# Kernel tuning notes

Measured on AMD Instinct MI355X. Metric: run time of the kernel, lower is better.

Reference implementation:

```python
import jax, jax.numpy as jnp
import numpy as np

N_NODES = 87381  # complete 4-ary tree of depth 9: (4**9 - 1) / 3
VOCAB = 32000
D_IN = 256
M_DIM = 256


def setup_inputs() -> dict:
    key = jax.random.key(0)
    ks = jax.random.split(key, 10)
    w = lambda k, s: jax.random.normal(k, s, dtype=jnp.float32) * 0.05
    return {
        "tokens": jax.random.randint(ks[0], (N_NODES,), 0, VOCAB),
        "branching": 4,
        "emb": w(ks[1], (VOCAB, D_IN)),
        "Wioux": w(ks[2], (D_IN, 3 * M_DIM)),
        "bioux": w(ks[3], (3 * M_DIM,)),
        "Wiouh": w(ks[4], (M_DIM, 3 * M_DIM)),
        "biouh": w(ks[5], (3 * M_DIM,)),
        "Wfx": w(ks[6], (D_IN, M_DIM)),
        "bfx": w(ks[7], (M_DIM,)),
        "Wfh": w(ks[8], (M_DIM, M_DIM)),
        "bfh": w(ks[9], (M_DIM,)),
    }


def _levels(n, b):
    # BFS level boundaries (start, size) for a complete b-ary tree with n nodes
    out, start, size = [], 0, 1
    while start < n:
        out.append((start, min(size, n - start)))
        start += size
        size *= b
    return out


def reference(tokens, branching, emb, Wioux, bioux, Wiouh, biouh, Wfx, bfx, Wfh, bfh):
    N = tokens.shape[0]
    b = int(branching)
    M = Wfh.shape[0]
    x = emb[tokens]                       # [N, D_IN] per-node inputs
    xiou = x @ Wioux + bioux              # [N, 3M] precomputed input gate terms
    xf = x @ Wfx + bfx                    # [N, M]
    h = jnp.zeros((N, M), x.dtype)
    c = jnp.zeros((N, M), x.dtype)
    for (s, sz) in reversed(_levels(N, b)):  # leaves -> root
        idx = jnp.arange(s, s + sz)
        child = idx[:, None] * b + 1 + jnp.arange(b)[None, :]   # [sz, b]
        valid = (child < N)[..., None].astype(x.dtype)          # [sz, b, 1]
        ci = jnp.where(child < N, child, 0)
        ch = h[ci] * valid                                      # [sz, b, M]
        cc = c[ci] * valid
        iou = xiou[idx] + ch.sum(axis=1) @ Wiouh + biouh        # [sz, 3M]
        i, o, u = jnp.split(iou, 3, axis=1)
        i, o, u = jax.nn.sigmoid(i), jax.nn.sigmoid(o), jnp.tanh(u)
        f = jax.nn.sigmoid(ch @ Wfh + bfh + xf[idx][:, None, :])  # [sz, b, M]
        c_new = i * u + jnp.sum(f * cc * valid, axis=1)
        h_new = o * jnp.tanh(c_new)
        c = c.at[idx].set(c_new)
        h = h.at[idx].set(h_new)
    return h  # hidden state of every node; root state is h[0]
```

## Files before the change

kernel.cpp:

```cpp
#include <hip/hip_runtime.h>
#include <cstdint>
#include <cstddef>

typedef _Float16 f16;
typedef __attribute__((ext_vector_type(8))) _Float16 half8;
typedef __attribute__((ext_vector_type(4))) _Float16 half4;
typedef __attribute__((ext_vector_type(8))) short short8;
typedef __attribute__((ext_vector_type(4))) float floatx4;
typedef __attribute__((ext_vector_type(8))) float floatx8;

__device__ __forceinline__ float rcp_(float x) { return __builtin_amdgcn_rcpf(x); }
__device__ __forceinline__ float sigm(float x) { return rcp_(1.f + __expf(-x)); }
__device__ __forceinline__ float tanh_(float x) { return 1.f - 2.f * rcp_(1.f + __expf(2.f * x)); }

__global__ __launch_bounds__(256) void gemm128d(
    const f16* __restrict__ A0, const f16* __restrict__ B0, f16* __restrict__ C0,
    int ldc0, int nt0, int tiles0,
    const f16* __restrict__ A1, const f16* __restrict__ B1, f16* __restrict__ C1,
    int ldc1, int nt1)
{
  const f16* A; const f16* BT; f16* C; int ldc_, mi, ni;
  int bid = blockIdx.x;
  if (bid < tiles0) { A = A0; BT = B0; C = C0; ldc_ = ldc0; mi = bid / nt0; ni = bid % nt0; }
  else { int r = bid - tiles0; A = A1; BT = B1; C = C1; ldc_ = ldc1; mi = r / nt1; ni = r % nt1; }
  const int m0 = mi * 128;
  const int n0 = ni * 128;

  __shared__ short lA[128 * 72];
  __shared__ short lB[128 * 72];
  const int t = threadIdx.x;
  const int wave = t >> 6;
  const int lane = t & 63;
  const int ln = lane & 15;
  const int quad = lane >> 4;
  const int wr = wave >> 1;
  const int wc = wave & 1;

  floatx4 acc[4][4];
#pragma unroll
  for (int i = 0; i < 4; ++i)
#pragma unroll
    for (int j = 0; j < 4; ++j) acc[i][j] = (floatx4){0.f, 0.f, 0.f, 0.f};

#pragma unroll
  for (int st = 0; st < 4; ++st) {
    const int k0 = st * 64;
#pragma unroll
    for (int i = 0; i < 4; ++i) {
      int chunk = t + 256 * i;
      int row = chunk >> 3;
      int cc = chunk & 7;
      *(short8*)&lA[row * 72 + cc * 8] =
          *(const short8*)(A + (size_t)(m0 + row) * 256 + k0 + cc * 8);
      *(short8*)&lB[row * 72 + cc * 8] =
          *(const short8*)(BT + (size_t)(n0 + row) * 256 + k0 + cc * 8);
    }
    __syncthreads();
#pragma unroll
    for (int ks = 0; ks < 2; ++ks) {
      const int kk = ks * 32 + quad * 8;
      half8 a[4], b[4];
#pragma unroll
      for (int rf = 0; rf < 4; ++rf)
        a[rf] = __builtin_bit_cast(half8,
            *(const short8*)&lA[(wr * 64 + rf * 16 + ln) * 72 + kk]);
#pragma unroll
      for (int cf = 0; cf < 4; ++cf)
        b[cf] = __builtin_bit_cast(half8,
            *(const short8*)&lB[(wc * 64 + cf * 16 + ln) * 72 + kk]);
#pragma unroll
      for (int rf = 0; rf < 4; ++rf)
#pragma unroll
        for (int cf = 0; cf < 4; ++cf)
          acc[rf][cf] = __builtin_amdgcn_mfma_f32_16x16x32_f16(
              a[rf], b[cf], acc[rf][cf], 0, 0, 0);
    }
    __syncthreads();
  }
#pragma unroll
  for (int rf = 0; rf < 4; ++rf)
#pragma unroll
    for (int cf = 0; cf < 4; ++cf)
#pragma unroll
      for (int r = 0; r < 4; ++r) {
        int row = m0 + wr * 64 + rf * 16 + quad * 4 + r;
        int col = n0 + wc * 64 + cf * 16 + ln;
        C[(size_t)row * ldc_ + col] = (f16)acc[rf][cf][r];
      }
}

__global__ __launch_bounds__(256) void prep(
    const float* __restrict__ emb, const float* __restrict__ Wioux,
    const float* __restrict__ Wfx, const float* __restrict__ Wiouh,
    const float* __restrict__ Wfh,
    f16* __restrict__ emb_h, f16* __restrict__ BTX,
    f16* __restrict__ WiouhT, f16* __restrict__ WfhT)
{
  int idx = blockIdx.x * 256 + threadIdx.x;
  if (idx < 2048000) {
    floatx4 v = *(const floatx4*)(emb + 4 * (size_t)idx);
    half4 o;
#pragma unroll
    for (int j = 0; j < 4; ++j) o[j] = (f16)v[j];
    *(half4*)(emb_h + 4 * (size_t)idx) = o;
  } else if (idx < 2310144) {
    int r = idx - 2048000;
    int j = r >> 8, k = r & 255;
    BTX[r] = (f16)((j < 768) ? Wioux[(size_t)k * 768 + j]
                             : Wfx[(size_t)k * 256 + (j - 768)]);
  } else if (idx < 2506752) {
    int r = idx - 2310144;
    int j = r >> 8, k = r & 255;
    WiouhT[r] = (f16)Wiouh[(size_t)k * 768 + j];
  } else {
    int r = idx - 2506752;
    int j = r >> 8, k = r & 255;
    WfhT[r] = (f16)Wfh[(size_t)k * 256 + j];
  }
}

__global__ __launch_bounds__(256) void elem8(
    const int* __restrict__ tokens, const f16* __restrict__ TIOUF,
    const f16* __restrict__ IOUH, const f16* __restrict__ FH,
    const float* __restrict__ bioux, const float* __restrict__ biouh,
    const float* __restrict__ bfx, const float* __restrict__ bfh,
    f16* __restrict__ c16, float* __restrict__ h, f16* __restrict__ h16,
    f16* __restrict__ hsum16, int s, int sz, int s_up, int sz_up, int leaf)
{
  __shared__ float hsh[8 * 260];
  const int t = threadIdx.x;
  const int nloc = t >> 5;
  const int d0 = (t & 31) * 8;
  const int base = s + 8 * blockIdx.x;
  const int node = base + nloc;
  const int lim = s + sz;

  if (node < lim) {
    const f16* ti = TIOUF + (size_t)tokens[node] * 1024;
    half8 t0 = *(const half8*)(ti + d0);
    half8 t1 = *(const half8*)(ti + 256 + d0);
    half8 t2 = *(const half8*)(ti + 512 + d0);
    floatx8 bi0 = *(const floatx8*)(bioux + d0) + *(const floatx8*)(biouh + d0);
    floatx8 bi1 = *(const floatx8*)(bioux + 256 + d0) + *(const floatx8*)(biouh + 256 + d0);
    floatx8 bi2 = *(const floatx8*)(bioux + 512 + d0) + *(const floatx8*)(biouh + 512 + d0);

    float cv[8];
    if (leaf) {
#pragma unroll
      for (int j = 0; j < 8; ++j)
        cv[j] = sigm((float)t0[j] + bi0[j]) * tanh_((float)t2[j] + bi2[j]);
    } else {
      const f16* io = IOUH + (size_t)(node - s) * 768;
      half8 io0 = *(const half8*)(io + d0);
      half8 io1 = *(const half8*)(io + 256 + d0);
      half8 io2 = *(const half8*)(io + 512 + d0);
      half8 t3 = *(const half8*)(ti + 768 + d0);
      floatx8 bff = *(const floatx8*)(bfx + d0) + *(const floatx8*)(bfh + d0);
      size_t ch = 4 * (size_t)node + 1;
      half8 fh0 = *(const half8*)(FH + (ch + 0) * 256 + d0);
      half8 fh1 = *(const half8*)(FH + (ch + 1) * 256 + d0);
      half8 fh2 = *(const half8*)(FH + (ch + 2) * 256 + d0);
      half8 fh3 = *(const half8*)(FH + (ch + 3) * 256 + d0);
      half8 cc0 = *(const half8*)(c16 + (ch + 0) * 256 + d0);
      half8 cc1 = *(const half8*)(c16 + (ch + 1) * 256 + d0);
      half8 cc2 = *(const half8*)(c16 + (ch + 2) * 256 + d0);
      half8 cc3 = *(const half8*)(c16 + (ch + 3) * 256 + d0);
#pragma unroll
      for (int j = 0; j < 8; ++j) {
        float xff = (float)t3[j] + bff[j];
        float v = sigm((float)t0[j] + (float)io0[j] + bi0[j]) *
                  tanh_((float)t2[j] + (float)io2[j] + bi2[j]);
        v += sigm((float)fh0[j] + xff) * (float)cc0[j];
        v += sigm((float)fh1[j] + xff) * (float)cc1[j];
        v += sigm((float)fh2[j] + xff) * (float)cc2[j];
        v += sigm((float)fh3[j] + xff) * (float)cc3[j];
        cv[j] = v;
      }
      t1 = __builtin_bit_cast(half8,
           __builtin_bit_cast(short8, t1));
#pragma unroll
      for (int j = 0; j < 8; ++j) bi1[j] += (float)io1[j];
    }

    half8 c8, h8;
    floatx8 hf;
#pragma unroll
    for (int j = 0; j < 8; ++j) {
      float hv = sigm((float)t1[j] + bi1[j]) * tanh_(cv[j]);
      c8[j] = (f16)cv[j];
      h8[j] = (f16)hv;
      hf[j] = hv;
    }
    *(half8*)(c16 + (size_t)node * 256 + d0) = c8;
    *(floatx8*)(h + (size_t)node * 256 + d0) = hf;
    *(half8*)(h16 + (size_t)node * 256 + d0) = h8;
    *(floatx8*)&hsh[nloc * 260 + d0] = hf;
  }
  __syncthreads();

  if (s_up >= 0 && t < 64) {
    int p = t >> 5;
    int dd = (t & 31) * 8;
    int parent = ((base - 1) >> 2) + p;
    if (parent < s_up + sz_up) {
      floatx8 v = *(const floatx8*)&hsh[(4 * p + 0) * 260 + dd] +
                  *(const floatx8*)&hsh[(4 * p + 1) * 260 + dd] +
                  *(const floatx8*)&hsh[(4 * p + 2) * 260 + dd] +
                  *(const floatx8*)&hsh[(4 * p + 3) * 260 + dd];
      half8 o;
#pragma unroll
      for (int j = 0; j < 8; ++j) o[j] = (f16)v[j];
      *(half8*)(hsum16 + (size_t)(parent - s_up) * 256 + dd) = o;
    }
  }
}

extern "C" void kernel_launch(void* const* d_in, const int* in_sizes, int n_in,
                              void* d_out, int out_size, void* d_ws, size_t ws_size,
                              hipStream_t stream) {
  const int*   tokens = (const int*)d_in[0];
  const float* emb    = (const float*)d_in[2];
  const float* Wioux  = (const float*)d_in[3];
  const float* bioux  = (const float*)d_in[4];
  const float* Wiouh  = (const float*)d_in[5];
  const float* biouh  = (const float*)d_in[6];
  const float* Wfx    = (const float*)d_in[7];
  const float* bfx    = (const float*)d_in[8];
  const float* Wfh    = (const float*)d_in[9];
  const float* bfh    = (const float*)d_in[10];
  float* h = (float*)d_out;
  (void)in_sizes; (void)n_in; (void)out_size; (void)ws_size;

  f16* emb_h   = (f16*)d_ws;
  f16* BTX     = emb_h   + 8192000;
  f16* WiouhT  = BTX     + 262144;
  f16* WfhT    = WiouhT  + 196608;
  f16* TIOUF   = WfhT    + 65536;
  f16* IOUH    = TIOUF   + (size_t)32768000;
  f16* FH      = IOUH    + (size_t)12582912;
  f16* h16     = FH      + (size_t)22396928;
  f16* hsum16  = h16     + (size_t)22396928;
  f16* c16     = hsum16  + (size_t)4194304;

  prep<<<10049, 256, 0, stream>>>(emb, Wioux, Wfx, Wiouh, Wfh,
                                  emb_h, BTX, WiouhT, WfhT);

  gemm128d<<<2000, 256, 0, stream>>>(emb_h, BTX, TIOUF, 1024, 8, 2000,
                                     emb_h, BTX, TIOUF, 1024, 8);

  const int LV[9][2] = {{21845, 65536}, {5461, 16384}, {1365, 4096},
                        {341, 1024},    {85, 256},     {21, 64},
                        {5, 16},        {1, 4},        {0, 1}};

  elem8<<<8192, 256, 0, stream>>>(tokens, TIOUF, nullptr, nullptr,
                                  bioux, biouh, bfx, bfh,
                                  c16, h, h16, hsum16, 21845, 65536, 5461, 16384, 1);

  for (int i = 1; i < 9; ++i) {
    int ps = LV[i - 1][0], psz = LV[i - 1][1];
    int s = LV[i][0], sz = LV[i][1];
    int mt0 = (psz + 127) / 128;
    int mt1 = (sz + 127) / 128;
    int tiles0 = mt0 * 2;
    int total = tiles0 + mt1 * 6;
    gemm128d<<<total, 256, 0, stream>>>(
        h16 + (size_t)ps * 256, WfhT, FH + (size_t)ps * 256, 256, 2, tiles0,
        hsum16, WiouhT, IOUH, 768, 6);
    int s_up = (i < 8) ? LV[i + 1][0] : -1;
    int sz_up = (i < 8) ? LV[i + 1][1] : 0;
    int blocks = (sz + 7) / 8;
    elem8<<<blocks, 256, 0, stream>>>(tokens, TIOUF, IOUH, FH,
                                      bioux, biouh, bfx, bfh,
                                      c16, h, h16, hsum16, s, sz, s_up, sz_up, 0);
  }
}
```

Measured before the change: 414.5 us.

## Fuse per-level recurrent GEMMs and gate elementwise into one MFMA kernel

```diff
diff --git a/kernel.cpp b/kernel.cpp
--- a/kernel.cpp
+++ b/kernel.cpp
@@ -215,6 +215,121 @@
   }
 }
 
+__global__ __launch_bounds__(512) void fused_level(
+    const int* __restrict__ tokens, const f16* __restrict__ TIOUF,
+    const f16* __restrict__ WiouhT, const f16* __restrict__ WfhT,
+    const float* __restrict__ bioux, const float* __restrict__ biouh,
+    const float* __restrict__ bfx, const float* __restrict__ bfh,
+    f16* __restrict__ c16, float* __restrict__ h, f16* __restrict__ h16,
+    const f16* __restrict__ hsum_in, f16* __restrict__ hsum_out,
+    int s, int sz, int sz_up)
+{
+  __shared__ short lA[80 * 264];
+  __shared__ float lFS[8][16][17];
+  __shared__ int ltok[16];
+
+  const int t = threadIdx.x;
+  const int pt = blockIdx.x >> 1;
+  const int pg = blockIdx.x & 1;
+  const int p0 = s + pt * 16;
+  const int c0 = 4 * p0 + 1;
+
+  if (t < 16) ltok[t] = tokens[p0 + t];
+#pragma unroll
+  for (int i = 0; i < 5; ++i) {
+    int chunk = t + 512 * i;
+    int row = chunk >> 5;
+    int cc = chunk & 31;
+    const f16* src = (row < 16)
+        ? hsum_in + (size_t)(pt * 16 + row) * 256 + cc * 8
+        : h16 + (size_t)(c0 + row - 16) * 256 + cc * 8;
+    *(short8*)&lA[row * 264 + cc * 8] = *(const short8*)src;
+  }
+  __syncthreads();
+
+  const int wave = t >> 6;
+  const int lane = t & 63;
+  const int ln = lane & 15;
+  const int q = lane >> 4;
+  const int dim = (pg * 8 + wave) * 16 + ln;
+
+  floatx4 accI[3], accF[4];
+#pragma unroll
+  for (int i = 0; i < 3; ++i) accI[i] = (floatx4){0.f, 0.f, 0.f, 0.f};
+#pragma unroll
+  for (int i = 0; i < 4; ++i) accF[i] = (floatx4){0.f, 0.f, 0.f, 0.f};
+
+  const short* aH = &lA[ln * 264 + 8 * q];
+  const short* aC = &lA[(16 + ln) * 264 + 8 * q];
+  const f16* b0p = WiouhT + (size_t)dim * 256 + 8 * q;
+  const f16* b1p = WiouhT + (size_t)(256 + dim) * 256 + 8 * q;
+  const f16* b2p = WiouhT + (size_t)(512 + dim) * 256 + 8 * q;
+  const f16* bfp = WfhT + (size_t)dim * 256 + 8 * q;
+
+#pragma unroll
+  for (int ks = 0; ks < 8; ++ks) {
+    const int ko = 32 * ks;
+    half8 ah = __builtin_bit_cast(half8, *(const short8*)(aH + ko));
+    half8 b0 = *(const half8*)(b0p + ko);
+    half8 b1 = *(const half8*)(b1p + ko);
+    half8 b2 = *(const half8*)(b2p + ko);
+    half8 bf = *(const half8*)(bfp + ko);
+    accI[0] = __builtin_amdgcn_mfma_f32_16x16x32_f16(ah, b0, accI[0], 0, 0, 0);
+    accI[1] = __builtin_amdgcn_mfma_f32_16x16x32_f16(ah, b1, accI[1], 0, 0, 0);
+    accI[2] = __builtin_amdgcn_mfma_f32_16x16x32_f16(ah, b2, accI[2], 0, 0, 0);
+#pragma unroll
+    for (int rt = 0; rt < 4; ++rt) {
+      half8 ac = __builtin_bit_cast(half8,
+          *(const short8*)(aC + rt * (16 * 264) + ko));
+      accF[rt] = __builtin_amdgcn_mfma_f32_16x16x32_f16(ac, bf, accF[rt], 0, 0, 0);
+    }
+  }
+
+  const float bi0 = bioux[dim] + biouh[dim];
+  const float bi1 = bioux[256 + dim] + biouh[256 + dim];
+  const float bi2 = bioux[512 + dim] + biouh[512 + dim];
+  const float bff = bfx[dim] + bfh[dim];
+
+#pragma unroll
+  for (int rt = 0; rt < 4; ++rt) {
+    int po = 4 * rt + q;
+    float xff = (float)TIOUF[(size_t)ltok[po] * 1024 + 768 + dim] + bff;
+    float fs = 0.f;
+#pragma unroll
+    for (int r = 0; r < 4; ++r) {
+      size_t child = (size_t)(c0 + 16 * rt + 4 * q + r);
+      fs += sigm(accF[rt][r] + xff) * (float)c16[child * 256 + dim];
+    }
+    lFS[wave][po][ln] = fs;
+  }
+  __syncthreads();
+
+  const int szrem = sz - pt * 16;
+  float hsum = 0.f;
+#pragma unroll
+  for (int r = 0; r < 4; ++r) {
+    int po = 4 * q + r;
+    const f16* tp = TIOUF + (size_t)ltok[po] * 1024;
+    float iv = sigm(accI[0][r] + (float)tp[dim] + bi0);
+    float ov = sigm(accI[1][r] + (float)tp[256 + dim] + bi1);
+    float uv = tanh_(accI[2][r] + (float)tp[512 + dim] + bi2);
+    float cn = iv * uv + lFS[wave][po][ln];
+    float hn = ov * tanh_(cn);
+    hsum += hn;
+    if (po < szrem) {
+      size_t pi = (size_t)(p0 + po);
+      c16[pi * 256 + dim] = (f16)cn;
+      h16[pi * 256 + dim] = (f16)hn;
+      h[pi * 256 + dim] = hn;
+    }
+  }
+  if (hsum_out) {
+    int g_row = 4 * pt + q;
+    if (g_row < sz_up)
+      hsum_out[(size_t)g_row * 256 + dim] = (f16)hsum;
+  }
+}
+
 extern "C" void kernel_launch(void* const* d_in, const int* in_sizes, int n_in,
                               void* d_out, int out_size, void* d_ws, size_t ws_size,
                               hipStream_t stream) {
@@ -236,11 +351,11 @@
   f16* WiouhT  = BTX     + 262144;
   f16* WfhT    = WiouhT  + 196608;
   f16* TIOUF   = WfhT    + 65536;
-  f16* IOUH    = TIOUF   + (size_t)32768000;
-  f16* FH      = IOUH    + (size_t)12582912;
-  f16* h16     = FH      + (size_t)22396928;
-  f16* hsum16  = h16     + (size_t)22396928;
-  f16* c16     = hsum16  + (size_t)4194304;
+  f16* hsumB   = TIOUF   + (size_t)32768000;
+  f16* FH_dead = hsumB   + (size_t)12582912;
+  f16* h16     = FH_dead + (size_t)22396928;
+  f16* hsumA   = h16     + (size_t)22396928;
+  f16* c16     = hsumA   + (size_t)4194304;
 
   prep<<<10049, 256, 0, stream>>>(emb, Wioux, Wfx, Wiouh, Wfh,
                                   emb_h, BTX, WiouhT, WfhT);
@@ -254,23 +369,16 @@
 
   elem8<<<8192, 256, 0, stream>>>(tokens, TIOUF, nullptr, nullptr,
                                   bioux, biouh, bfx, bfh,
-                                  c16, h, h16, hsum16, 21845, 65536, 5461, 16384, 1);
+                                  c16, h, h16, hsumA, 21845, 65536, 5461, 16384, 1);
 
   for (int i = 1; i < 9; ++i) {
-    int ps = LV[i - 1][0], psz = LV[i - 1][1];
     int s = LV[i][0], sz = LV[i][1];
-    int mt0 = (psz + 127) / 128;
-    int mt1 = (sz + 127) / 128;
-    int tiles0 = mt0 * 2;
-    int total = tiles0 + mt1 * 6;
-    gemm128d<<<total, 256, 0, stream>>>(
-        h16 + (size_t)ps * 256, WfhT, FH + (size_t)ps * 256, 256, 2, tiles0,
-        hsum16, WiouhT, IOUH, 768, 6);
-    int s_up = (i < 8) ? LV[i + 1][0] : -1;
     int sz_up = (i < 8) ? LV[i + 1][1] : 0;
-    int blocks = (sz + 7) / 8;
-    elem8<<<blocks, 256, 0, stream>>>(tokens, TIOUF, IOUH, FH,
-                                      bioux, biouh, bfx, bfh,
-                                      c16, h, h16, hsum16, s, sz, s_up, sz_up, 0);
-  }
-}
+    const f16* hin = (i & 1) ? hsumA : hsumB;
+    f16* hout = (i < 8) ? ((i & 1) ? hsumB : hsumA) : nullptr;
+    int blocks = 2 * ((sz + 15) / 16);
+    fused_level<<<blocks, 512, 0, stream>>>(
+        tokens, TIOUF, WiouhT, WfhT, bioux, biouh, bfx, bfh,
+        c16, h, h16, hin, hout, s, sz, sz_up);
+  }
+}
```

Measured after the change: 387.5 us. 6.5% less time.
